# Performance work log

Hardware: AMD Instinct MI355X
Metric: run time of the kernel (lower is better)

Reference implementation:

```python
import jax, jax.numpy as jnp
import numpy as np

B, N, DIM = 4, 2048, 512
HEADS, DIM_HEAD = 8, 64
HIDDEN = HEADS * DIM_HEAD  # == DIM


def _rotary(t):
    # t: [b, h, n, d]; interleaved rotary (rotary-embedding-torch style), theta=10000
    n, d = t.shape[-2], t.shape[-1]
    inv_freq = 1.0 / (10000.0 ** (jnp.arange(0, d, 2, dtype=jnp.float32) / d))  # [d/2]
    freqs = jnp.arange(n, dtype=jnp.float32)[:, None] * inv_freq[None, :]        # [n, d/2]
    freqs = jnp.repeat(freqs, 2, axis=-1)                                        # [n, d]
    cos, sin = jnp.cos(freqs), jnp.sin(freqs)
    x1, x2 = t[..., ::2], t[..., 1::2]
    rot = jnp.stack((-x2, x1), axis=-1).reshape(t.shape)  # rotate_half, interleaved
    return t * cos + rot * sin


def setup_inputs() -> dict:
    key = jax.random.key(0)
    k1, k2, k3, k4 = jax.random.split(key, 4)
    x = jax.random.normal(k1, (B, N, DIM), dtype=jnp.float32)
    pos_bias = jax.random.normal(k2, (HEADS, N, N), dtype=jnp.float32)
    W_qkv = jax.random.normal(k3, (DIM, 3 * HIDDEN), dtype=jnp.float32) * (DIM ** -0.5)
    W_out = jax.random.normal(k4, (HIDDEN, DIM), dtype=jnp.float32) * (HIDDEN ** -0.5)
    return {"x": x, "pos_bias": pos_bias, "W_qkv": W_qkv, "W_out": W_out}


def reference(x, pos_bias, W_qkv, W_out):
    b, n, _ = x.shape
    qkv = x @ W_qkv                                   # [b, n, 3*h*d]
    q, k, v = jnp.split(qkv, 3, axis=-1)

    def to_heads(t):
        return t.reshape(b, n, HEADS, DIM_HEAD).transpose(0, 2, 1, 3)  # [b,h,n,d]

    q = to_heads(q) * (DIM_HEAD ** -0.5)
    k = to_heads(k)
    v = to_heads(v)
    q = _rotary(q)
    k = _rotary(k)
    sim = jnp.einsum('bhid,bhjd->bhij', q, k) + pos_bias[None]  # [b,h,n,n]
    attn = jax.nn.softmax(sim, axis=-1)                          # stable softmax (== amax-subtract + softmax)
    out = jnp.einsum('bhij,bhjd->bhid', attn, v)
    out = out.transpose(0, 2, 1, 3).reshape(b, n, HIDDEN)
    return out @ W_out
```

## Files before the change

### kernel.cpp

```cpp
#include <hip/hip_runtime.h>
#include <hip/hip_bf16.h>

#define DEV static __device__ __forceinline__

typedef __attribute__((ext_vector_type(8))) short s16x8;
typedef __attribute__((ext_vector_type(16))) float f32x16;

DEV float bf2f(short s) {
    unsigned u = ((unsigned)(unsigned short)s) << 16;
    union { unsigned u; float f; } c; c.u = u; return c.f;
}
DEV short f2bf(float f) {
    union { float f; unsigned u; } c; c.f = f;
    unsigned u = c.u;
    unsigned r = (u + 0x7FFFu + ((u >> 16) & 1u)) >> 16;
    return (short)r;
}

DEV f32x16 mfma(s16x8 a, s16x8 b, f32x16 c) {
    return __builtin_amdgcn_mfma_f32_32x32x16_bf16(a, b, c, 0, 0, 0);
}

__global__ void cvt_f32_bf16(const float* __restrict__ src,
                             short* __restrict__ dst, int n) {
    int i = (blockIdx.x * blockDim.x + threadIdx.x) * 4;
    if (i >= n) return;
    float4 v = *(const float4*)(src + i);
    short4 o;
    o.x = f2bf(v.x); o.y = f2bf(v.y); o.z = f2bf(v.z); o.w = f2bf(v.w);
    *(short4*)(dst + i) = o;
}

__global__ void rotab(float2* __restrict__ tab) {
    int idx = blockIdx.x * 256 + threadIdx.x;
    int n = idx >> 5, f = idx & 31;
    float inv = expf(-0.2878231366f * (float)f);
    float a = (float)n * inv;
    tab[idx] = make_float2(cosf(a), sinf(a));
}

__global__ void ktransf(const float* __restrict__ src, short* __restrict__ dst,
                        int R, int C) {
    __shared__ __align__(16) short t[32][33];
    int tx = threadIdx.x & 31, ty = threadIdx.x >> 5;
    int r0 = blockIdx.y * 32, c0 = blockIdx.x * 32;
    for (int i = 0; i < 32; i += 8)
        t[ty + i][tx] = f2bf(src[(size_t)(r0 + ty + i) * C + c0 + tx]);
    __syncthreads();
    for (int i = 0; i < 32; i += 8)
        dst[(size_t)(c0 + ty + i) * R + r0 + tx] = t[tx][ty + i];
}

__global__ __launch_bounds__(256) void gemm_qkv(
    const short* __restrict__ X, const short* __restrict__ WT,
    const float2* __restrict__ rtab,
    short* __restrict__ qws, short* __restrict__ kws, short* __restrict__ vt) {
    int wave = threadIdx.x >> 6, lane = threadIdx.x & 63;
    int l31 = lane & 31, lh = lane >> 5;
    int mw = blockIdx.x * 128 + (wave >> 1) * 64;
    int nw = blockIdx.y * 128 + (wave & 1) * 64;
    f32x16 acc[2][2] = {};
    const short* ap = X + (size_t)(mw + l31) * 512 + lh * 8;
    const short* bp = WT + (size_t)(nw + l31) * 512 + lh * 8;
#pragma unroll 4
    for (int k = 0; k < 512; k += 16) {
        s16x8 a0 = *(const s16x8*)(ap + k);
        s16x8 a1 = *(const s16x8*)(ap + 32 * 512 + k);
        s16x8 b0 = *(const s16x8*)(bp + k);
        s16x8 b1 = *(const s16x8*)(bp + 32 * 512 + k);
        acc[0][0] = mfma(a0, b0, acc[0][0]);
        acc[0][1] = mfma(a0, b1, acc[0][1]);
        acc[1][0] = mfma(a1, b0, acc[1][0]);
        acc[1][1] = mfma(a1, b1, acc[1][1]);
    }
#pragma unroll
    for (int ib = 0; ib < 2; ib++)
#pragma unroll
        for (int jb = 0; jb < 2; jb++) {
            int col = nw + jb * 32 + l31;
            int t = col >> 9;
            int cid = col & 511;
            int h = cid >> 6, d = cid & 63;
#pragma unroll
            for (int r = 0; r < 16; r++) {
                int row = (r & 3) + 8 * (r >> 2) + 4 * lh;
                int gm = mw + ib * 32 + row;
                int b = gm >> 11, n = gm & 2047;
                float v = acc[ib][jb][r];
                if (t == 0) v *= 0.125f;
                if (t < 2) {
                    float pv = __shfl_xor(v, 1);
                    float2 cs = rtab[n * 32 + (d >> 1)];
                    float o = (d & 1) ? (v * cs.x + pv * cs.y)
                                      : (v * cs.x - pv * cs.y);
                    short* dst = (t == 0) ? qws : kws;
                    dst[((size_t)(b * 8 + h) * 2048 + n) * 64 + d] = f2bf(o);
                } else {
                    vt[((size_t)(b * 8 + h) * 64 + d) * 2048 + n] = f2bf(v);
                }
            }
        }
}

#define PROW 72
__global__ __launch_bounds__(64, 3) void attn(
    const short* __restrict__ qws, const short* __restrict__ kws,
    const short* __restrict__ vt, const float* __restrict__ bias,
    short* __restrict__ ows) {
    __shared__ __align__(16) short pls[32 * PROW];
    int lane = threadIdx.x;
    int l31 = lane & 31, lh = lane >> 5;
    int bh = blockIdx.y;
    int b = bh >> 3, h = bh & 7;
    int q0 = blockIdx.x * 32;

    const short* qp = qws + ((size_t)bh * 2048 + q0 + l31) * 64 + lh * 8;
    s16x8 qf[4];
#pragma unroll
    for (int c = 0; c < 4; c++) qf[c] = *(const s16x8*)(qp + c * 16);

    f32x16 oa[2] = {};
    float lsum[16];
#pragma unroll
    for (int r = 0; r < 16; r++) lsum[r] = 0.f;
    short* pw = &pls[0];
    const float* bias_base = bias + ((size_t)h * 2048 + q0) * 2048;

    for (int kt = 0; kt < 32; kt++) {
        int kb = kt * 64;
        float bf0[16], bf1[16];
#pragma unroll
        for (int r = 0; r < 16; r++) {
            int row = (r & 3) + 8 * (r >> 2) + 4 * lh;
            const float* bp = bias_base + (size_t)row * 2048 + kb;
            bf0[r] = bp[l31];
            bf1[r] = bp[32 + l31];
        }
        const short* kp = kws + ((size_t)bh * 2048 + kb + l31) * 64 + lh * 8;
        f32x16 s0 = {}, s1 = {};
#pragma unroll
        for (int c = 0; c < 4; c++) {
            s16x8 k0 = *(const s16x8*)(kp + c * 16);
            s16x8 k1 = *(const s16x8*)(kp + 32 * 64 + c * 16);
            s0 = mfma(qf[c], k0, s0);
            s1 = mfma(qf[c], k1, s1);
        }
#pragma unroll
        for (int r = 0; r < 16; r++) {
            int row = (r & 3) + 8 * (r >> 2) + 4 * lh;
            float e0 = __expf(s0[r] + bf0[r]);
            float e1 = __expf(s1[r] + bf1[r]);
            lsum[r] += e0 + e1;
            pw[row * PROW + l31] = f2bf(e0);
            pw[row * PROW + 32 + l31] = f2bf(e1);
        }
        const short* vp = vt + ((size_t)bh * 64 + l31) * 2048 + kb + lh * 8;
#pragma unroll
        for (int c = 0; c < 4; c++) {
            s16x8 pf = *(const s16x8*)(pw + l31 * PROW + c * 16 + lh * 8);
            s16x8 v0f = *(const s16x8*)(vp + c * 16);
            s16x8 v1f = *(const s16x8*)(vp + (size_t)32 * 2048 + c * 16);
            oa[0] = mfma(pf, v0f, oa[0]);
            oa[1] = mfma(pf, v1f, oa[1]);
        }
    }
#pragma unroll
    for (int r = 0; r < 16; r++) {
        float s = lsum[r];
#pragma unroll
        for (int off = 16; off >= 1; off >>= 1)
            s += __shfl_xor(s, off);
        float inv = 1.f / s;
        int row = (r & 3) + 8 * (r >> 2) + 4 * lh;
        size_t o0 = ((size_t)(b * 2048 + q0 + row) * 8 + h) * 64;
        ows[o0 + l31] = f2bf(oa[0][r] * inv);
        ows[o0 + 32 + l31] = f2bf(oa[1][r] * inv);
    }
}

__global__ __launch_bounds__(256) void gemm_out(
    const short* __restrict__ O, const short* __restrict__ WT,
    float* __restrict__ out) {
    int wave = threadIdx.x >> 6, lane = threadIdx.x & 63;
    int l31 = lane & 31, lh = lane >> 5;
    int m0 = blockIdx.x * 128 + (wave >> 1) * 64;
    int n0 = blockIdx.y * 128 + (wave & 1) * 64;
    f32x16 acc[2][2] = {};
    const short* ap = O + (size_t)(m0 + l31) * 512 + lh * 8;
    const short* bp = WT + (size_t)(n0 + l31) * 512 + lh * 8;
#pragma unroll 4
    for (int k = 0; k < 512; k += 16) {
        s16x8 a0 = *(const s16x8*)(ap + k);
        s16x8 a1 = *(const s16x8*)(ap + 32 * 512 + k);
        s16x8 b0 = *(const s16x8*)(bp + k);
        s16x8 b1 = *(const s16x8*)(bp + 32 * 512 + k);
        acc[0][0] = mfma(a0, b0, acc[0][0]);
        acc[0][1] = mfma(a0, b1, acc[0][1]);
        acc[1][0] = mfma(a1, b0, acc[1][0]);
        acc[1][1] = mfma(a1, b1, acc[1][1]);
    }
#pragma unroll
    for (int ib = 0; ib < 2; ib++)
#pragma unroll
        for (int jb = 0; jb < 2; jb++)
#pragma unroll
            for (int r = 0; r < 16; r++) {
                int row = (r & 3) + 8 * (r >> 2) + 4 * lh;
                out[(size_t)(m0 + ib * 32 + row) * 512 + n0 + jb * 32 + l31] =
                    acc[ib][jb][r];
            }
}

extern "C" void kernel_launch(void* const* d_in, const int* in_sizes, int n_in,
                              void* d_out, int out_size, void* d_ws,
                              size_t ws_size, hipStream_t stream) {
    const float* x    = (const float*)d_in[0];
    const float* bias = (const float*)d_in[1];
    const float* wqkv = (const float*)d_in[2];
    const float* wout = (const float*)d_in[3];
    float* out = (float*)d_out;

    char* ws = (char*)d_ws;
    short* xbf   = (short*)ws;
    short* wqkvT = xbf + 4194304;
    short* woutT = wqkvT + 786432;
    short* qws   = woutT + 262144;
    short* kws   = qws + 4194304;
    short* vt    = kws + 4194304;
    short* ows   = vt + 4194304;
    float2* rtab = (float2*)(ows + 4194304);

    cvt_f32_bf16<<<4096, 256, 0, stream>>>(x, xbf, 4194304);
    rotab<<<256, 256, 0, stream>>>(rtab);
    ktransf<<<dim3(1536 / 32, 512 / 32), 256, 0, stream>>>(wqkv, wqkvT, 512, 1536);
    ktransf<<<dim3(512 / 32, 512 / 32), 256, 0, stream>>>(wout, woutT, 512, 512);
    gemm_qkv<<<dim3(64, 12), 256, 0, stream>>>(xbf, wqkvT, rtab, qws, kws, vt);
    attn<<<dim3(64, 32), 64, 0, stream>>>(qws, kws, vt, bias, ows);
    gemm_out<<<dim3(64, 4), 256, 0, stream>>>(ows, woutT, out);
}
```

Measured before the change: 442.9 us.

## Double-buffer pos_bias tiles into LDS via async global_load_lds and swizzle P

The attention kernel now prefetches the next 32x64 fp32 pos_bias tile straight into a double-buffered LDS array with global_load_lds. The copy overlaps the QK^T MFMAs and the current tile's exp work, replacing per-lane strided scalar global loads. K fragments are loaded up front and fenced with sched barriers and an explicit vmcnt wait. The P staging buffer drops its padding in favour of an XOR swizzle against bank conflicts. The larger LDS footprint and the removed occupancy hint may lower waves per CU, and the hand-written vmcnt count must match the number of outstanding loads.

```diff
diff --git a/kernel.cpp b/kernel.cpp
--- a/kernel.cpp
+++ b/kernel.cpp
@@ -19,6 +19,12 @@
 
 DEV f32x16 mfma(s16x8 a, s16x8 b, f32x16 c) {
     return __builtin_amdgcn_mfma_f32_32x32x16_bf16(a, b, c, 0, 0, 0);
+}
+
+typedef const __attribute__((address_space(1))) unsigned gu32;
+typedef __attribute__((address_space(3))) unsigned lu32;
+DEV void gll16(const float* g, float* l) {
+    __builtin_amdgcn_global_load_lds((gu32*)g, (lu32*)l, 16, 0, 0);
 }
 
 __global__ void cvt_f32_bf16(const float* __restrict__ src,
@@ -102,12 +108,12 @@
         }
 }
 
-#define PROW 72
-__global__ __launch_bounds__(64, 3) void attn(
+__global__ __launch_bounds__(64) void attn(
     const short* __restrict__ qws, const short* __restrict__ kws,
     const short* __restrict__ vt, const float* __restrict__ bias,
     short* __restrict__ ows) {
-    __shared__ __align__(16) short pls[32 * PROW];
+    __shared__ __align__(16) short pls[32 * 64];
+    __shared__ __align__(16) float blds[2][32][64];
     int lane = threadIdx.x;
     int l31 = lane & 31, lh = lane >> 5;
     int bh = blockIdx.y;
@@ -124,40 +130,56 @@
 #pragma unroll
     for (int r = 0; r < 16; r++) lsum[r] = 0.f;
     short* pw = &pls[0];
-    const float* bias_base = bias + ((size_t)h * 2048 + q0) * 2048;
+
+    const float* bbase = bias + ((size_t)h * 2048 + q0) * 2048;
+    int grow = lane >> 4;
+    int gcol = (lane & 15) * 4;
+
+#pragma unroll
+    for (int j = 0; j < 8; j++)
+        gll16(bbase + (size_t)(4 * j + grow) * 2048 + gcol, &blds[0][4 * j][0]);
 
     for (int kt = 0; kt < 32; kt++) {
         int kb = kt * 64;
-        float bf0[16], bf1[16];
+        int p = kt & 1;
+        const short* kp = kws + ((size_t)bh * 2048 + kb + l31) * 64 + lh * 8;
+        s16x8 k0[4], k1[4];
+#pragma unroll
+        for (int c = 0; c < 4; c++) {
+            k0[c] = *(const s16x8*)(kp + c * 16);
+            k1[c] = *(const s16x8*)(kp + 32 * 64 + c * 16);
+        }
+        __builtin_amdgcn_sched_barrier(0);
+        if (kt < 31) {
+            const float* bnx = bbase + (size_t)(kt + 1) * 64;
+#pragma unroll
+            for (int j = 0; j < 8; j++)
+                gll16(bnx + (size_t)(4 * j + grow) * 2048 + gcol,
+                      &blds[p ^ 1][4 * j][0]);
+        }
+        f32x16 s0 = {}, s1 = {};
+#pragma unroll
+        for (int c = 0; c < 4; c++) {
+            s0 = mfma(qf[c], k0[c], s0);
+            s1 = mfma(qf[c], k1[c], s1);
+        }
+        asm volatile("s_waitcnt vmcnt(16)" ::: "memory");
+        __builtin_amdgcn_sched_barrier(0);
 #pragma unroll
         for (int r = 0; r < 16; r++) {
             int row = (r & 3) + 8 * (r >> 2) + 4 * lh;
-            const float* bp = bias_base + (size_t)row * 2048 + kb;
-            bf0[r] = bp[l31];
-            bf1[r] = bp[32 + l31];
-        }
-        const short* kp = kws + ((size_t)bh * 2048 + kb + l31) * 64 + lh * 8;
-        f32x16 s0 = {}, s1 = {};
+            float e0 = __expf(s0[r] + blds[p][row][l31]);
+            float e1 = __expf(s1[r] + blds[p][row][32 + l31]);
+            lsum[r] += e0 + e1;
+            int sw = (row & 7) << 3;
+            pw[row * 64 + (l31 ^ sw)] = f2bf(e0);
+            pw[row * 64 + ((32 + l31) ^ sw)] = f2bf(e1);
+        }
+        const short* vp = vt + ((size_t)bh * 64 + l31) * 2048 + kb + lh * 8;
 #pragma unroll
         for (int c = 0; c < 4; c++) {
-            s16x8 k0 = *(const s16x8*)(kp + c * 16);
-            s16x8 k1 = *(const s16x8*)(kp + 32 * 64 + c * 16);
-            s0 = mfma(qf[c], k0, s0);
-            s1 = mfma(qf[c], k1, s1);
-        }
-#pragma unroll
-        for (int r = 0; r < 16; r++) {
-            int row = (r & 3) + 8 * (r >> 2) + 4 * lh;
-            float e0 = __expf(s0[r] + bf0[r]);
-            float e1 = __expf(s1[r] + bf1[r]);
-            lsum[r] += e0 + e1;
-            pw[row * PROW + l31] = f2bf(e0);
-            pw[row * PROW + 32 + l31] = f2bf(e1);
-        }
-        const short* vp = vt + ((size_t)bh * 64 + l31) * 2048 + kb + lh * 8;
-#pragma unroll
-        for (int c = 0; c < 4; c++) {
-            s16x8 pf = *(const s16x8*)(pw + l31 * PROW + c * 16 + lh * 8);
+            s16x8 pf = *(const s16x8*)(
+                pw + l31 * 64 + ((c * 16 + lh * 8) ^ ((l31 & 7) << 3)));
             s16x8 v0f = *(const s16x8*)(vp + c * 16);
             s16x8 v1f = *(const s16x8*)(vp + (size_t)32 * 2048 + c * 16);
             oa[0] = mfma(pf, v0f, oa[0]);
```

Measured after the change: 423.2 us. -4.5%, faster.
